# Kernel tuning notes

Measured on AMD Instinct MI355X. Metric: run time of the kernel, lower is better.

The kernel has to match this reference:

```python
import jax, jax.numpy as jnp
import numpy as np
from jax import lax

C = 128          # channel_size
NUM_HEAD = 2
P = 4            # local_patch_num


def setup_inputs() -> dict:
    key = jax.random.key(0)
    ks = jax.random.split(key, 16)
    def w(k, shape, scale=0.02):
        return jax.random.normal(k, shape, dtype=jnp.float32) * scale
    return dict(
        x=jax.random.normal(ks[0], (16, C, 128, 128), jnp.float32),
        h0=jax.random.normal(ks[1], (1, C, 64, 64), jnp.float32),
        c0=jax.random.normal(ks[2], (1, C, 64, 64), jnp.float32),
        conv_w=w(ks[3], (C, C, 2, 2)), conv_b=jnp.zeros((C,), jnp.float32),
        qkv1_w=w(ks[4], (3 * C, C)), qkv1_b=jnp.zeros((3 * C,), jnp.float32),
        mlp1_w1=w(ks[5], (4 * C, C)), mlp1_b1=jnp.zeros((4 * C,), jnp.float32),
        mlp1_w2=w(ks[6], (C, 4 * C)), mlp1_b2=jnp.zeros((C,), jnp.float32),
        qkv2_w=w(ks[7], (3 * C, C)), qkv2_b=jnp.zeros((3 * C,), jnp.float32),
        mlp2_w1=w(ks[8], (4 * C, C)), mlp2_b1=jnp.zeros((4 * C,), jnp.float32),
        mlp2_w2=w(ks[9], (C, 4 * C)), mlp2_b2=jnp.zeros((C,), jnp.float32),
        lstm_wx=w(ks[10], (4 * C, C)),   # 1x1 conv, no bias
        lstm_wh=w(ks[11], (4 * C, C)),   # 1x1 conv
        lstm_bh=jnp.zeros((4 * C,), jnp.float32),
    )


def _linear(x, w, b):
    # torch Linear: y = x @ W.T + b, W is [out, in]
    return jnp.einsum('...i,oi->...o', x, w) + b


def _msa(x, w, b, num_head):
    # x: [b, A, L, c]; attend over L within each group A. scale = sqrt(channel_size).
    bb, A, L, c = x.shape
    hd = c // num_head
    qkv = _linear(x, w, b).reshape(bb, A, L, 3, num_head, hd)
    q = jnp.transpose(qkv[..., 0, :, :], (0, 1, 3, 2, 4))  # [b,A,h,L,hd]
    k = jnp.transpose(qkv[..., 1, :, :], (0, 1, 3, 2, 4))
    v = jnp.transpose(qkv[..., 2, :, :], (0, 1, 3, 2, 4))
    score = jnp.einsum('bahlc,bahmc->bahlm', q, k) / (c ** 0.5)
    attn = jax.nn.softmax(score, axis=-1)
    out = jnp.einsum('bahlm,bahmc->bahlc', attn, v)
    return jnp.transpose(out, (0, 1, 3, 2, 4)).reshape(bb, A, L, c)


def _mlp(x, w1, b1, w2, b2):
    return _linear(jax.nn.gelu(_linear(x, w1, b1), approximate=False), w2, b2)


def reference(x, h0, c0, conv_w, conv_b,
              qkv1_w, qkv1_b, mlp1_w1, mlp1_b1, mlp1_w2, mlp1_b2,
              qkv2_w, qkv2_b, mlp2_w1, mlp2_b1, mlp2_w2, mlp2_b2,
              lstm_wx, lstm_wh, lstm_bh):
    # Conv2d(C, C, kernel=2, stride=2)
    x = lax.conv_general_dilated(x, conv_w, (2, 2), 'VALID',
                                 dimension_numbers=('NCHW', 'OIHW', 'NCHW'))
    x = x + conv_b[None, :, None, None]
    b, c, Hs, Ws = x.shape
    yg, xg = Hs // P, Ws // P
    # Window_partition: b c (yg yl) (xg xl) -> b (yg xg) (yl xl) c
    xw = x.reshape(b, c, yg, P, xg, P).transpose(0, 2, 4, 3, 5, 1).reshape(b, yg * xg, P * P, c)
    xw = xw + _msa(xw, qkv1_w, qkv1_b, NUM_HEAD)      # LocalMSA over window tokens
    xw = xw + _mlp(xw, mlp1_w1, mlp1_b1, mlp1_w2, mlp1_b2)
    xt = jnp.transpose(xw, (0, 2, 1, 3))              # b g l c -> b l g c
    xt = xt + _msa(xt, qkv2_w, qkv2_b, NUM_HEAD)      # DilatedMSA over windows
    xt = xt + _mlp(xt, mlp2_w1, mlp2_b1, mlp2_w2, mlp2_b2)
    # Window_reverse: b (yl xl) (yg xg) c -> b c (yg yl) (xg xl)
    xr = xt.reshape(b, P, P, yg, xg, c).transpose(0, 5, 3, 1, 4, 2).reshape(b, c, yg * P, xg * P)

    # ConvLSTM recurrence over the batch dimension (hidden carried sample-to-sample)
    def step(carry, xi):
        h, Cc = carry  # [C,H,W]
        gates = (jnp.einsum('oc,chw->ohw', lstm_wx, xi)
                 + jnp.einsum('oc,chw->ohw', lstm_wh, h)
                 + lstm_bh[:, None, None])
        f, i, s, o = jnp.split(gates, 4, axis=0)
        f = jax.nn.softmax(f, axis=0)   # Softmax2d = softmax over channels
        i = jax.nn.softmax(i, axis=0)
        o = jax.nn.softmax(o, axis=0)
        s = jnp.tanh(s)
        Cn = f * Cc + i * s
        hn = o * jnp.tanh(Cn)
        return (hn, Cn), hn

    (hf, Cf), hs = lax.scan(step, (h0[0], c0[0]), xr)
    return hs, hf[None], Cf[None]
```

## Files before the change

kernel.cpp:

```cpp
#include <hip/hip_runtime.h>
#include <hip/hip_bf16.h>

typedef unsigned int u32;
typedef unsigned short u16;

#define DI __device__ __forceinline__

typedef __attribute__((ext_vector_type(8))) __bf16 bf16x8;
typedef __attribute__((ext_vector_type(4))) float f32x4;

DI float b2f_u(u32 u){ return __uint_as_float(u << 16); }
DI u16 f2b_u(float f){
  u32 x = __float_as_uint(f);
  x += 0x7fffu + ((x >> 16) & 1u);
  return (u16)(x >> 16);
}
DI void ld8b(const u16* p, float* o){
  uint4 v = *reinterpret_cast<const uint4*>(p);
  o[0] = b2f_u(v.x & 0xffffu); o[1] = b2f_u(v.x >> 16);
  o[2] = b2f_u(v.y & 0xffffu); o[3] = b2f_u(v.y >> 16);
  o[4] = b2f_u(v.z & 0xffffu); o[5] = b2f_u(v.z >> 16);
  o[6] = b2f_u(v.w & 0xffffu); o[7] = b2f_u(v.w >> 16);
}
DI void st8b(u16* p, const float* i){
  uint4 v;
  v.x = (u32)f2b_u(i[0]) | ((u32)f2b_u(i[1]) << 16);
  v.y = (u32)f2b_u(i[2]) | ((u32)f2b_u(i[3]) << 16);
  v.z = (u32)f2b_u(i[4]) | ((u32)f2b_u(i[5]) << 16);
  v.w = (u32)f2b_u(i[6]) | ((u32)f2b_u(i[7]) << 16);
  *reinterpret_cast<uint4*>(p) = v;
}

__global__ void k_detect(const u32* __restrict__ xw, int* __restrict__ flag){
  __shared__ int cnt;
  int t = threadIdx.x;
  if (t == 0) cnt = 0;
  __syncthreads();
  int c = 0;
  for (int i = t; i < 2048; i += 256){
    u32 lo = xw[i] & 0xffffu;
    u32 e = (lo >> 7) & 0xffu;
    if (e < 100u || e > 140u) c++;
  }
  atomicAdd(&cnt, c);
  __syncthreads();
  if (t == 0) *flag = (cnt > 200) ? 1 : 0;
}

__global__ void k_prep(
  const void* __restrict__ conv_w, const void* __restrict__ qkv1_w,
  const void* __restrict__ m1w1, const void* __restrict__ m1w2,
  const void* __restrict__ qkv2_w, const void* __restrict__ m2w1, const void* __restrict__ m2w2,
  const void* __restrict__ lwx, const void* __restrict__ lwh,
  const void* __restrict__ conv_b, const void* __restrict__ qkv1_b,
  const void* __restrict__ m1b1, const void* __restrict__ m1b2,
  const void* __restrict__ qkv2_b, const void* __restrict__ m2b1, const void* __restrict__ m2b2,
  const void* __restrict__ lbh,
  u16* __restrict__ wB_conv, u16* __restrict__ wB_qkv1, u16* __restrict__ wB_m1a,
  u16* __restrict__ wB_m1b, u16* __restrict__ wB_qkv2, u16* __restrict__ wB_m2a,
  u16* __restrict__ wB_m2b, u16* __restrict__ wBx, u16* __restrict__ wBh,
  float* __restrict__ bf_conv, float* __restrict__ bf_qkv1, float* __restrict__ bf_m1b1,
  float* __restrict__ bf_m1b2, float* __restrict__ bf_qkv2, float* __restrict__ bf_m2b1,
  float* __restrict__ bf_m2b2, float* __restrict__ bf_lbh,
  const int* __restrict__ flag){
  int bid = blockIdx.x, t = threadIdx.x;
  int fl = *flag;
  auto cvb = [&](const void* s, u16* d, int base, int n){
    int i = (bid - base)*256 + t;
    if (i < n) d[i] = fl ? f2b_u(((const float*)s)[i]) : ((const u16*)s)[i];
  };
  auto ldf = [&](const void* s, int i)->float{
    return fl ? ((const float*)s)[i] : b2f_u((u32)((const u16*)s)[i]);
  };
  if (bid < 256)       cvb(conv_w, wB_conv, 0,    65536);
  else if (bid < 448)  cvb(qkv1_w, wB_qkv1, 256,  49152);
  else if (bid < 704)  cvb(m1w1,   wB_m1a,  448,  65536);
  else if (bid < 960)  cvb(m1w2,   wB_m1b,  704,  65536);
  else if (bid < 1152) cvb(qkv2_w, wB_qkv2, 960,  49152);
  else if (bid < 1408) cvb(m2w1,   wB_m2a,  1152, 65536);
  else if (bid < 1664) cvb(m2w2,   wB_m2b,  1408, 65536);
  else if (bid < 1920) cvb(lwx,    wBx,     1664, 65536);
  else if (bid < 2176) cvb(lwh,    wBh,     1920, 65536);
  else {
    int i = (bid - 2176)*256 + t;
    if (i < 128)       bf_conv[i]        = ldf(conv_b, i);
    else if (i < 512)  bf_qkv1[i-128]    = ldf(qkv1_b, i-128);
    else if (i < 1024) bf_m1b1[i-512]    = ldf(m1b1,   i-512);
    else if (i < 1152) bf_m1b2[i-1024]   = ldf(m1b2,   i-1024);
    else if (i < 1536) bf_qkv2[i-1152]   = ldf(qkv2_b, i-1152);
    else if (i < 2048) bf_m2b1[i-1536]   = ldf(m2b1,   i-1536);
    else if (i < 2176) bf_m2b2[i-2048]   = ldf(m2b2,   i-2048);
    else if (i < 2688) bf_lbh[i-2176]    = ldf(lbh,    i-2176);
  }
}

__global__ __launch_bounds__(256) void k_conv(const void* __restrict__ x_raw,
                                              const u16* __restrict__ wB,
                                              const float* __restrict__ bias, u16* __restrict__ outA,
                                              const int* __restrict__ flag){
  __shared__ __align__(16) u16 pool[128*136];
  u16* Aa = pool;
  u16* Ys = pool;
  int t = threadIdx.x, bid = blockIdx.x;
  int xh = bid & 1, yg = (bid >> 1) & 15, b = bid >> 5;
  size_t slab = (size_t)b*2097152 + (size_t)(yg*8)*128 + (size_t)xh*64;
  int w = t >> 6, lane = t & 63, fr = lane & 15, fg = lane >> 4;
  f32x4 acc[2][8];
  #pragma unroll
  for (int j=0;j<8;j++){
    float bv = bias[j*16 + fr];
    acc[0][j] = {bv,bv,bv,bv};
    acc[1][j] = {bv,bv,bv,bv};
  }
  for (int ci0 = 0; ci0 < 128; ci0 += 16){
    if (ci0) __syncthreads();
    if (*flag){
      const float* xb = (const float*)x_raw + slab + (size_t)ci0*16384;
      #pragma unroll
      for (int i=0;i<4;i++){
        int idx = i*256 + t;
        int row = idx >> 3, seg = idx & 7;
        int cr = row >> 3, py = row & 7;
        const float* sp = xb + (size_t)cr*16384 + py*128 + seg*8;
        float4 v0 = *reinterpret_cast<const float4*>(sp);
        float4 v1 = *reinterpret_cast<const float4*>(sp + 4);
        int tok0 = seg*16 + (py>>1)*4;
        int k0 = cr*4 + (py&1)*2;
        *reinterpret_cast<u32*>(&Aa[(tok0+0)*72 + k0]) = (u32)f2b_u(v0.x) | ((u32)f2b_u(v0.y)<<16);
        *reinterpret_cast<u32*>(&Aa[(tok0+1)*72 + k0]) = (u32)f2b_u(v0.z) | ((u32)f2b_u(v0.w)<<16);
        *reinterpret_cast<u32*>(&Aa[(tok0+2)*72 + k0]) = (u32)f2b_u(v1.x) | ((u32)f2b_u(v1.y)<<16);
        *reinterpret_cast<u32*>(&Aa[(tok0+3)*72 + k0]) = (u32)f2b_u(v1.z) | ((u32)f2b_u(v1.w)<<16);
      }
    } else {
      const u16* xb = (const u16*)x_raw + slab + (size_t)ci0*16384;
      #pragma unroll
      for (int i=0;i<4;i++){
        int idx = i*256 + t;
        int row = idx >> 3, seg = idx & 7;
        int cr = row >> 3, py = row & 7;
        uint4 v = *reinterpret_cast<const uint4*>(xb + (size_t)cr*16384 + py*128 + seg*8);
        int tok0 = seg*16 + (py>>1)*4;
        int k0 = cr*4 + (py&1)*2;
        *reinterpret_cast<u32*>(&Aa[(tok0+0)*72 + k0]) = v.x;
        *reinterpret_cast<u32*>(&Aa[(tok0+1)*72 + k0]) = v.y;
        *reinterpret_cast<u32*>(&Aa[(tok0+2)*72 + k0]) = v.z;
        *reinterpret_cast<u32*>(&Aa[(tok0+3)*72 + k0]) = v.w;
      }
    }
    __syncthreads();
    bf16x8 a0[2], a1[2];
    #pragma unroll
    for (int kk=0;kk<2;kk++){
      a0[kk] = *reinterpret_cast<const bf16x8*>(&Aa[(w*16+fr)*72 + kk*32 + fg*8]);
      a1[kk] = *reinterpret_cast<const bf16x8*>(&Aa[((w+4)*16+fr)*72 + kk*32 + fg*8]);
    }
    #pragma unroll
    for (int j=0;j<8;j++){
      const u16* wp = wB + (size_t)(j*16+fr)*512 + ci0*4 + fg*8;
      bf16x8 b0 = *reinterpret_cast<const bf16x8*>(wp);
      bf16x8 b1 = *reinterpret_cast<const bf16x8*>(wp + 32);
      acc[0][j] = __builtin_amdgcn_mfma_f32_16x16x32_bf16(a0[0], b0, acc[0][j], 0, 0, 0);
      acc[0][j] = __builtin_amdgcn_mfma_f32_16x16x32_bf16(a0[1], b1, acc[0][j], 0, 0, 0);
      acc[1][j] = __builtin_amdgcn_mfma_f32_16x16x32_bf16(a1[0], b0, acc[1][j], 0, 0, 0);
      acc[1][j] = __builtin_amdgcn_mfma_f32_16x16x32_bf16(a1[1], b1, acc[1][j], 0, 0, 0);
    }
  }
  __syncthreads();
  #pragma unroll
  for (int tt=0;tt<2;tt++){
    int tokbase = (w + tt*4)*16;
    #pragma unroll
    for (int j=0;j<8;j++){
      #pragma unroll
      for (int r=0;r<4;r++)
        Ys[(tokbase + fg*4 + r)*136 + j*16 + fr] = f2b_u(acc[tt][j][r]);
    }
  }
  __syncthreads();
  {
    int tok = t >> 1, half = t & 1;
    int gl = yg*16 + xh*8 + (tok >> 4);
    int l = tok & 15;
    u16* dst = outA + ((size_t)(b*256 + gl)*16 + l)*128 + half*64;
    const u16* src = &Ys[tok*136 + half*64];
    #pragma unroll
    for (int q2=0;q2<8;q2++)
      *reinterpret_cast<uint4*>(dst + q2*8) = *reinterpret_cast<const uint4*>(src + q2*8);
  }
}

__global__ __launch_bounds__(256) void k_msa1(const u16* __restrict__ A, const u16* __restrict__ wB,
                                              const float* __restrict__ qbias, u16* __restrict__ B){
  __shared__ u16 Xs[32*136];
  __shared__ float QKV[32*388];
  __shared__ float S[1024];
  int t = threadIdx.x, bid = blockIdx.x;
  {
    int l = t >> 3, c0 = (t & 7)*16;
    const u16* src = A + (size_t)bid*4096 + l*128 + c0;
    *reinterpret_cast<uint4*>(&Xs[l*136 + c0])     = *reinterpret_cast<const uint4*>(src);
    *reinterpret_cast<uint4*>(&Xs[l*136 + c0 + 8]) = *reinterpret_cast<const uint4*>(src + 8);
  }
  __syncthreads();
  {
    int w = t >> 6, lane = t & 63, fr = lane & 15, fg = lane >> 4;
    bf16x8 a0[4], a1[4];
    #pragma unroll
    for (int k=0;k<4;k++){
      a0[k] = *reinterpret_cast<const bf16x8*>(&Xs[fr*136 + k*32 + fg*8]);
      a1[k] = *reinterpret_cast<const bf16x8*>(&Xs[(16+fr)*136 + k*32 + fg*8]);
    }
    #pragma unroll
    for (int j=0;j<6;j++){
      int o = w*96 + j*16 + fr;
      float bv = qbias[o];
      f32x4 d0 = {bv,bv,bv,bv}, d1 = {bv,bv,bv,bv};
      const u16* wp = wB + (size_t)o*128 + fg*8;
      #pragma unroll
      for (int k=0;k<4;k++){
        bf16x8 b = *reinterpret_cast<const bf16x8*>(wp + k*32);
        d0 = __builtin_amdgcn_mfma_f32_16x16x32_bf16(a0[k], b, d0, 0, 0, 0);
        d1 = __builtin_amdgcn_mfma_f32_16x16x32_bf16(a1[k], b, d1, 0, 0, 0);
      }
      #pragma unroll
      for (int r=0;r<4;r++){
        QKV[(fg*4+r)*388 + o]      = d0[r];
        QKV[(16+fg*4+r)*388 + o]   = d1[r];
      }
    }
  }
  __syncthreads();
  const float scale = 0.08838834764831845f;
  for (int e = t; e < 1024; e += 256){
    int win = e >> 9, h = (e>>8)&1, l = (e>>4)&15, m = e&15;
    const float* q = &QKV[(win*16+l)*388 + h*64];
    const float* kk = &QKV[(win*16+m)*388 + 128 + h*64];
    float s = 0.f;
    #pragma unroll
    for (int d=0; d<64; d++) s += q[d]*kk[d];
    S[win*512 + (h*16+l)*16 + m] = s*scale;
  }
  __syncthreads();
  if (t < 64){
    float* row = &S[(t>>5)*512 + (t&31)*16];
    float mx = row[0];
    #pragma unroll
    for (int m=1;m<16;m++) mx = fmaxf(mx,row[m]);
    float sum = 0.f;
    #pragma unroll
    for (int m=0;m<16;m++){ float e = expf(row[m]-mx); row[m]=e; sum+=e; }
    float inv = 1.0f/sum;
    #pragma unroll
    for (int m=0;m<16;m++) row[m] *= inv;
  }
  __syncthreads();
  {
    int l32 = t >> 3, og = t & 7, o0 = og*16;
    int win = l32 >> 4, l = l32 & 15;
    float out16[16];
    #pragma unroll
    for (int j=0;j<16;j++){
      int o = o0+j, h = o >> 6, d = o & 63;
      const float* p = &S[win*512 + (h*16+l)*16];
      float s = 0.f;
      #pragma unroll
      for (int m=0;m<16;m++) s += p[m]*QKV[(win*16+m)*388 + 256 + h*64 + d];
      out16[j] = s + b2f_u((u32)Xs[l32*136 + o]);
    }
    st8b(B + (size_t)bid*4096 + l32*128 + o0, out16);
    st8b(B + (size_t)bid*4096 + l32*128 + o0 + 8, out16 + 8);
  }
}

template<int MODE>
__global__ __launch_bounds__(256) void k_mlp(const u16* __restrict__ in,
    const u16* __restrict__ w1B, const float* __restrict__ b1,
    const u16* __restrict__ w2B, const float* __restrict__ b2,
    u16* __restrict__ out){
  __shared__ u16 Xs[32*136];
  __shared__ u16 Hs[32*520];
  __shared__ u16 Ys[32*136];
  int t = threadIdx.x, bid = blockIdx.x;
  {
    int l = t >> 3, c0 = (t & 7)*16;
    const u16* src = in + (size_t)bid*4096 + l*128 + c0;
    *reinterpret_cast<uint4*>(&Xs[l*136 + c0])     = *reinterpret_cast<const uint4*>(src);
    *reinterpret_cast<uint4*>(&Xs[l*136 + c0 + 8]) = *reinterpret_cast<const uint4*>(src + 8);
  }
  __syncthreads();
  int w = t >> 6, lane = t & 63, fr = lane & 15, fg = lane >> 4;

  {
    bf16x8 a0[4], a1[4];
    #pragma unroll
    for (int k=0;k<4;k++){
      a0[k] = *reinterpret_cast<const bf16x8*>(&Xs[fr*136 + k*32 + fg*8]);
      a1[k] = *reinterpret_cast<const bf16x8*>(&Xs[(16+fr)*136 + k*32 + fg*8]);
    }
    #pragma unroll
    for (int j=0;j<8;j++){
      int o = w*128 + j*16 + fr;
      float bv = b1[o];
      f32x4 d0 = {bv,bv,bv,bv}, d1 = {bv,bv,bv,bv};
      const u16* wp = w1B + (size_t)o*128 + fg*8;
      #pragma unroll
      for (int k=0;k<4;k++){
        bf16x8 b = *reinterpret_cast<const bf16x8*>(wp + k*32);
        d0 = __builtin_amdgcn_mfma_f32_16x16x32_bf16(a0[k], b, d0, 0, 0, 0);
        d1 = __builtin_amdgcn_mfma_f32_16x16x32_bf16(a1[k], b, d1, 0, 0, 0);
      }
      #pragma unroll
      for (int r=0;r<4;r++){
        float v0 = d0[r], v1 = d1[r];
        Hs[(fg*4+r)*520 + o]      = f2b_u(0.5f*v0*(1.0f + erff(v0*0.70710678118654752f)));
        Hs[(16+fg*4+r)*520 + o]   = f2b_u(0.5f*v1*(1.0f + erff(v1*0.70710678118654752f)));
      }
    }
  }
  __syncthreads();

  {
    int na = w*32 + fr, nb = na + 16;
    float ba = b2[na], bb = b2[nb];
    f32x4 d00 = {ba,ba,ba,ba}, d01 = {bb,bb,bb,bb};
    f32x4 d10 = {ba,ba,ba,ba}, d11 = {bb,bb,bb,bb};
    const u16* wpa = w2B + (size_t)na*512 + fg*8;
    const u16* wpb = w2B + (size_t)nb*512 + fg*8;
    #pragma unroll
    for (int k=0;k<16;k++){
      bf16x8 aa = *reinterpret_cast<const bf16x8*>(&Hs[fr*520 + k*32 + fg*8]);
      bf16x8 ab = *reinterpret_cast<const bf16x8*>(&Hs[(16+fr)*520 + k*32 + fg*8]);
      bf16x8 bA = *reinterpret_cast<const bf16x8*>(wpa + k*32);
      bf16x8 bB = *reinterpret_cast<const bf16x8*>(wpb + k*32);
      d00 = __builtin_amdgcn_mfma_f32_16x16x32_bf16(aa, bA, d00, 0, 0, 0);
      d01 = __builtin_amdgcn_mfma_f32_16x16x32_bf16(aa, bB, d01, 0, 0, 0);
      d10 = __builtin_amdgcn_mfma_f32_16x16x32_bf16(ab, bA, d10, 0, 0, 0);
      d11 = __builtin_amdgcn_mfma_f32_16x16x32_bf16(ab, bB, d11, 0, 0, 0);
    }
    #pragma unroll
    for (int r=0;r<4;r++){
      int ta = fg*4 + r, tb = 16 + ta;
      Ys[ta*136 + na] = f2b_u(d00[r] + b2f_u((u32)Xs[ta*136 + na]));
      Ys[ta*136 + nb] = f2b_u(d01[r] + b2f_u((u32)Xs[ta*136 + nb]));
      Ys[tb*136 + na] = f2b_u(d10[r] + b2f_u((u32)Xs[tb*136 + na]));
      Ys[tb*136 + nb] = f2b_u(d11[r] + b2f_u((u32)Xs[tb*136 + nb]));
    }
  }
  __syncthreads();

  {
    int tok = t >> 3, oc = (t & 7)*16;
    uint4 v0 = *reinterpret_cast<const uint4*>(&Ys[tok*136 + oc]);
    uint4 v1 = *reinterpret_cast<const uint4*>(&Ys[tok*136 + oc + 8]);
    int T = bid*32 + tok;
    size_t addr;
    if (MODE == 1){
      int b = T >> 12, g = (T >> 4) & 255, ll = T & 15;
      addr = ((size_t)((b*16 + ll)*256 + g))*128 + oc;
    } else {
      int b = T >> 12, ll = (T >> 8) & 15, g = T & 255;
      int pcoord = ((g >> 4)*4 + (ll >> 2))*64 + ((g & 15)*4 + (ll & 3));
      addr = ((size_t)(b*4096 + pcoord))*128 + oc;
    }
    *reinterpret_cast<uint4*>(out + addr)     = v0;
    *reinterpret_cast<uint4*>(out + addr + 8) = v1;
  }
}

__global__ __launch_bounds__(256) void k_qkv2(const u16* __restrict__ in, const u16* __restrict__ wB,
                                              const float* __restrict__ bias,
                                              u16* __restrict__ qbuf, u16* __restrict__ kvbuf){
  __shared__ u16 Xs[32*136];
  __shared__ u16 Qs[32*392];
  int t = threadIdx.x, bid = blockIdx.x;
  {
    int l = t >> 3, c0 = (t & 7)*16;
    const u16* src = in + (size_t)bid*4096 + l*128 + c0;
    *reinterpret_cast<uint4*>(&Xs[l*136 + c0])     = *reinterpret_cast<const uint4*>(src);
    *reinterpret_cast<uint4*>(&Xs[l*136 + c0 + 8]) = *reinterpret_cast<const uint4*>(src + 8);
  }
  __syncthreads();
  {
    int w = t >> 6, lane = t & 63, fr = lane & 15, fg = lane >> 4;
    bf16x8 a0[4], a1[4];
    #pragma unroll
    for (int k=0;k<4;k++){
      a0[k] = *reinterpret_cast<const bf16x8*>(&Xs[fr*136 + k*32 + fg*8]);
      a1[k] = *reinterpret_cast<const bf16x8*>(&Xs[(16+fr)*136 + k*32 + fg*8]);
    }
    #pragma unroll
    for (int j=0;j<6;j++){
      int o = w*96 + j*16 + fr;
      float bv = bias[o];
      f32x4 d0 = {bv,bv,bv,bv}, d1 = {bv,bv,bv,bv};
      const u16* wp = wB + (size_t)o*128 + fg*8;
      #pragma unroll
      for (int k=0;k<4;k++){
        bf16x8 b = *reinterpret_cast<const bf16x8*>(wp + k*32);
        d0 = __builtin_amdgcn_mfma_f32_16x16x32_bf16(a0[k], b, d0, 0, 0, 0);
        d1 = __builtin_amdgcn_mfma_f32_16x16x32_bf16(a1[k], b, d1, 0, 0, 0);
      }
      #pragma unroll
      for (int r=0;r<4;r++){
        Qs[(fg*4+r)*392 + o]    = f2b_u(d0[r]);
        Qs[(16+fg*4+r)*392 + o] = f2b_u(d1[r]);
      }
    }
  }
  __syncthreads();
  {
    int l = t >> 3, og = t & 7, o0 = og*48;
    size_t tok = (size_t)bid*32 + l;
    #pragma unroll
    for (int m=0; m<6; m++){
      int oc = o0 + m*8;
      uint4 v = *reinterpret_cast<const uint4*>(&Qs[l*392 + oc]);
      if (oc < 128) *reinterpret_cast<uint4*>(qbuf + tok*128 + oc) = v;
      else          *reinterpret_cast<uint4*>(kvbuf + tok*256 + (oc-128)) = v;
    }
  }
}

__global__ __launch_bounds__(256) void k_attn2(const u16* __restrict__ qbuf, const u16* __restrict__ kvbuf,
                                               u16* __restrict__ y){
  __shared__ __align__(16) char pool[24064];
  u16* Qb = (u16*)pool;
  u16* Kb = (u16*)(pool + 9216);
  u16* Vt = (u16*)(pool + 13824);
  u16* Pb = (u16*)(pool + 18944);
  float* Os = (float*)pool;

  int t = threadIdx.x, bid = blockIdx.x;
  int qt = bid & 3, h = (bid >> 2) & 1, bl = bid >> 3;
  size_t tokbase = (size_t)bl * 256;
  {
    int r = t >> 2, seg = t & 3;
    const u16* src = qbuf + (tokbase + qt*64 + r)*128 + h*64 + seg*16;
    uint4 v0 = *reinterpret_cast<const uint4*>(src);
    uint4 v1 = *reinterpret_cast<const uint4*>(src + 8);
    *reinterpret_cast<uint4*>(&Qb[r*72 + seg*16])     = v0;
    *reinterpret_cast<uint4*>(&Qb[r*72 + seg*16 + 8]) = v1;
  }
  int w = t >> 6, lane = t & 63;
  int fc = lane & 15, fg = lane >> 4;
  float m_reg[4], l_reg[4];
  #pragma unroll
  for (int r=0;r<4;r++){ m_reg[r] = -1e30f; l_reg[r] = 0.0f; }
  f32x4 o[4];
  #pragma unroll
  for (int j=0;j<4;j++) o[j] = {0.f,0.f,0.f,0.f};
  const float scale = 0.08838834764831845f;

  for (int kt=0; kt<8; kt++){
    {
      int r = t >> 3, seg = t & 7;
      const u16* base = kvbuf + (tokbase + kt*32 + r)*256 + h*64;
      *reinterpret_cast<uint4*>(&Kb[r*72 + seg*8]) = *reinterpret_cast<const uint4*>(base + seg*8);
    }
    {
      int pp = t >> 4, dg = t & 15, d0 = dg*4;
      const u16* b0 = kvbuf + (tokbase + kt*32 + 2*pp)*256 + h*64 + 128 + d0;
      uint2 v0 = *reinterpret_cast<const uint2*>(b0);
      uint2 v1 = *reinterpret_cast<const uint2*>(b0 + 256);
      *reinterpret_cast<u32*>(&Vt[(d0+0)*40 + 2*pp]) = (v0.x & 0xffffu) | (v1.x << 16);
      *reinterpret_cast<u32*>(&Vt[(d0+1)*40 + 2*pp]) = (v0.x >> 16) | (v1.x & 0xffff0000u);
      *reinterpret_cast<u32*>(&Vt[(d0+2)*40 + 2*pp]) = (v0.y & 0xffffu) | (v1.y << 16);
      *reinterpret_cast<u32*>(&Vt[(d0+3)*40 + 2*pp]) = (v0.y >> 16) | (v1.y & 0xffff0000u);
    }
    __syncthreads();
    f32x4 s0 = {0.f,0.f,0.f,0.f}, s1 = {0.f,0.f,0.f,0.f};
    {
      bf16x8 a0  = *reinterpret_cast<const bf16x8*>(&Qb[(w*16+fc)*72 + fg*8]);
      bf16x8 a1  = *reinterpret_cast<const bf16x8*>(&Qb[(w*16+fc)*72 + 32 + fg*8]);
      bf16x8 b00 = *reinterpret_cast<const bf16x8*>(&Kb[fc*72 + fg*8]);
      bf16x8 b01 = *reinterpret_cast<const bf16x8*>(&Kb[fc*72 + 32 + fg*8]);
      bf16x8 b10 = *reinterpret_cast<const bf16x8*>(&Kb[(16+fc)*72 + fg*8]);
      bf16x8 b11 = *reinterpret_cast<const bf16x8*>(&Kb[(16+fc)*72 + 32 + fg*8]);
      s0 = __builtin_amdgcn_mfma_f32_16x16x32_bf16(a0, b00, s0, 0, 0, 0);
      s0 = __builtin_amdgcn_mfma_f32_16x16x32_bf16(a1, b01, s0, 0, 0, 0);
      s1 = __builtin_amdgcn_mfma_f32_16x16x32_bf16(a0, b10, s1, 0, 0, 0);
      s1 = __builtin_amdgcn_mfma_f32_16x16x32_bf16(a1, b11, s1, 0, 0, 0);
    }
    float corr[4];
    #pragma unroll
    for (int r=0;r<4;r++){
      float v0 = s0[r]*scale, v1 = s1[r]*scale;
      float mx = fmaxf(v0, v1);
      mx = fmaxf(mx, __shfl_xor(mx, 1));
      mx = fmaxf(mx, __shfl_xor(mx, 2));
      mx = fmaxf(mx, __shfl_xor(mx, 4));
      mx = fmaxf(mx, __shfl_xor(mx, 8));
      float mnew = fmaxf(m_reg[r], mx);
      corr[r] = expf(m_reg[r] - mnew);
      m_reg[r] = mnew;
      float p0 = expf(v0 - mnew), p1 = expf(v1 - mnew);
      float sum = p0 + p1;
      sum += __shfl_xor(sum, 1);
      sum += __shfl_xor(sum, 2);
      sum += __shfl_xor(sum, 4);
      sum += __shfl_xor(sum, 8);
      l_reg[r] = l_reg[r]*corr[r] + sum;
      int row = w*16 + fg*4 + r;
      Pb[row*40 + fc]      = f2b_u(p0);
      Pb[row*40 + 16 + fc] = f2b_u(p1);
    }
    {
      bf16x8 pa = *reinterpret_cast<const bf16x8*>(&Pb[(w*16+fc)*40 + fg*8]);
      #pragma unroll
      for (int jt=0;jt<4;jt++){
        bf16x8 vb = *reinterpret_cast<const bf16x8*>(&Vt[(jt*16+fc)*40 + fg*8]);
        f32x4 oo = o[jt];
        oo[0] *= corr[0]; oo[1] *= corr[1]; oo[2] *= corr[2]; oo[3] *= corr[3];
        o[jt] = __builtin_amdgcn_mfma_f32_16x16x32_bf16(pa, vb, oo, 0, 0, 0);
      }
    }
    __syncthreads();
  }
  float inv[4];
  #pragma unroll
  for (int r=0;r<4;r++) inv[r] = 1.0f / l_reg[r];
  #pragma unroll
  for (int jt=0;jt<4;jt++){
    #pragma unroll
    for (int r=0;r<4;r++)
      Os[(w*16 + fg*4 + r)*68 + jt*16 + fc] = o[jt][r] * inv[r];
  }
  __syncthreads();
  {
    int row = t >> 2, seg = t & 3;
    float ov[16];
    #pragma unroll
    for (int j=0;j<16;j++) ov[j] = Os[row*68 + seg*16 + j];
    u16* dst = y + (tokbase + qt*64 + row)*128 + h*64 + seg*16;
    float res[16]; ld8b(dst, res); ld8b(dst+8, res+8);
    float o16[16];
    #pragma unroll
    for (int j=0;j<16;j++) o16[j] = ov[j] + res[j];
    st8b(dst, o16); st8b(dst+8, o16+8);
  }
}

__global__ __launch_bounds__(512) void k_lstm_all(const u16* __restrict__ xD,
    const void* __restrict__ h0, const void* __restrict__ c0,
    const u16* __restrict__ wBx, const u16* __restrict__ wBh, const float* __restrict__ bh,
    void* __restrict__ dout, const int* __restrict__ flag){
  __shared__ u16 Xa[16*136];
  __shared__ u16 Ha[16*136];
  __shared__ float glds[4*16*132];
  __shared__ float part[4*16*132];
  __shared__ float Cls[16*132];
  __shared__ u16 hst[16*136];
  int t = threadIdx.x, bid = blockIdx.x;
  int pix0 = bid*16;
  int fl = *flag;
  if (t < 256){
    int c = t >> 1, half = t & 1;
    int pxb = half*8;
    if (fl){
      const float* hp = (const float*)h0 + (size_t)c*4096 + pix0 + pxb;
      const float* cp = (const float*)c0 + (size_t)c*4096 + pix0 + pxb;
      #pragma unroll
      for (int i=0;i<8;i++){
        Ha[(pxb+i)*136 + c] = f2b_u(hp[i]);
        Cls[(pxb+i)*132 + c] = cp[i];
      }
    } else {
      const u16* hp = (const u16*)h0 + (size_t)c*4096 + pix0 + pxb;
      const u16* cp = (const u16*)c0 + (size_t)c*4096 + pix0 + pxb;
      #pragma unroll
      for (int i=0;i<8;i++){
        Ha[(pxb+i)*136 + c] = hp[i];
        Cls[(pxb+i)*132 + c] = b2f_u((u32)cp[i]);
      }
    }
  }
  int w = t >> 6, lane = t & 63, fr = lane & 15, fg = lane >> 4;
  int g = w & 3, ks = w >> 2;
  const u16* wSel = ks ? wBh : wBx;
  const u16* aSel = ks ? Ha : Xa;
  for (int n = 0; n < 16; n++){
    if (t < 256){
      int px = t >> 4, c0v = (t & 15)*8;
      *reinterpret_cast<uint4*>(&Xa[px*136 + c0v]) =
        *reinterpret_cast<const uint4*>(xD + ((size_t)n*4096 + pix0 + px)*128 + c0v);
    }
    __syncthreads();
    f32x4 acc[8];
    {
      bf16x8 a[4];
      #pragma unroll
      for (int k=0;k<4;k++)
        a[k] = *reinterpret_cast<const bf16x8*>(&aSel[fr*136 + k*32 + fg*8]);
      #pragma unroll
      for (int j=0;j<8;j++){
        int o = g*128 + j*16 + fr;
        f32x4 d;
        if (ks == 0){ float bv = bh[o]; d = {bv,bv,bv,bv}; }
        else        { d = {0.f,0.f,0.f,0.f}; }
        const u16* wp = wSel + (size_t)o*128 + fg*8;
        #pragma unroll
        for (int k=0;k<4;k++){
          bf16x8 b = *reinterpret_cast<const bf16x8*>(wp + k*32);
          d = __builtin_amdgcn_mfma_f32_16x16x32_bf16(a[k], b, d, 0, 0, 0);
        }
        acc[j] = d;
      }
    }
    if (ks == 1){
      #pragma unroll
      for (int j=0;j<8;j++)
        #pragma unroll
        for (int r=0;r<4;r++)
          part[(g*16 + fg*4 + r)*132 + j*16 + fr] = acc[j][r];
    }
    __syncthreads();
    if (ks == 0){
      #pragma unroll
      for (int j=0;j<8;j++)
        #pragma unroll
        for (int r=0;r<4;r++)
          acc[j][r] += part[(g*16 + fg*4 + r)*132 + j*16 + fr];
      if (g == 2){
        #pragma unroll
        for (int j=0;j<8;j++)
          #pragma unroll
          for (int r=0;r<4;r++)
            glds[(g*16 + fg*4 + r)*132 + j*16 + fr] = tanhf(acc[j][r]);
      } else {
        #pragma unroll
        for (int r=0;r<4;r++){
          float mx = acc[0][r];
          #pragma unroll
          for (int j=1;j<8;j++) mx = fmaxf(mx, acc[j][r]);
          mx = fmaxf(mx, __shfl_xor(mx, 1));
          mx = fmaxf(mx, __shfl_xor(mx, 2));
          mx = fmaxf(mx, __shfl_xor(mx, 4));
          mx = fmaxf(mx, __shfl_xor(mx, 8));
          float e[8], sum = 0.f;
          #pragma unroll
          for (int j=0;j<8;j++){ e[j] = expf(acc[j][r] - mx); sum += e[j]; }
          sum += __shfl_xor(sum, 1);
          sum += __shfl_xor(sum, 2);
          sum += __shfl_xor(sum, 4);
          sum += __shfl_xor(sum, 8);
          float inv = 1.0f/sum;
          #pragma unroll
          for (int j=0;j<8;j++)
            glds[(g*16 + fg*4 + r)*132 + j*16 + fr] = e[j]*inv;
        }
      }
    }
    __syncthreads();
    if (t < 256){
      int chg = t & 15, px = t >> 4;
      int ch0 = chg*8;
      float fv[8], iv[8], sv[8], ov[8], cc[8];
      #pragma unroll
      for (int q2=0;q2<2;q2++){
        *reinterpret_cast<float4*>(&fv[q2*4]) = *reinterpret_cast<const float4*>(&glds[(0*16+px)*132 + ch0 + q2*4]);
        *reinterpret_cast<float4*>(&iv[q2*4]) = *reinterpret_cast<const float4*>(&glds[(1*16+px)*132 + ch0 + q2*4]);
        *reinterpret_cast<float4*>(&sv[q2*4]) = *reinterpret_cast<const float4*>(&glds[(2*16+px)*132 + ch0 + q2*4]);
        *reinterpret_cast<float4*>(&ov[q2*4]) = *reinterpret_cast<const float4*>(&glds[(3*16+px)*132 + ch0 + q2*4]);
        *reinterpret_cast<float4*>(&cc[q2*4]) = *reinterpret_cast<const float4*>(&Cls[px*132 + ch0 + q2*4]);
      }
      float cn[8], hn[8];
      #pragma unroll
      for (int j=0;j<8;j++){
        cn[j] = fv[j]*cc[j] + iv[j]*sv[j];
        hn[j] = ov[j]*tanhf(cn[j]);
      }
      #pragma unroll
      for (int q2=0;q2<2;q2++)
        *reinterpret_cast<float4*>(&Cls[px*132 + ch0 + q2*4]) = *reinterpret_cast<const float4*>(&cn[q2*4]);
      uint4 pk;
      pk.x = (u32)f2b_u(hn[0]) | ((u32)f2b_u(hn[1]) << 16);
      pk.y = (u32)f2b_u(hn[2]) | ((u32)f2b_u(hn[3]) << 16);
      pk.z = (u32)f2b_u(hn[4]) | ((u32)f2b_u(hn[5]) << 16);
      pk.w = (u32)f2b_u(hn[6]) | ((u32)f2b_u(hn[7]) << 16);
      *reinterpret_cast<uint4*>(&Ha[px*136 + ch0])  = pk;
      *reinterpret_cast<uint4*>(&hst[px*136 + ch0]) = pk;
      if (n == 15){
        #pragma unroll
        for (int q2=0;q2<2;q2++)
          *reinterpret_cast<float4*>(&glds[px*132 + ch0 + q2*4]) = *reinterpret_cast<const float4*>(&hn[q2*4]);
      }
    }
    __syncthreads();
    if (t < 256){
      int ch = t >> 1, ph = t & 1;
      size_t ob = (size_t)n*524288 + (size_t)ch*4096 + pix0 + ph*8;
      if (fl){
        float* df = (float*)dout;
        float v[8];
        #pragma unroll
        for (int i=0;i<8;i++) v[i] = b2f_u((u32)hst[(ph*8+i)*136 + ch]);
        *reinterpret_cast<float4*>(df + ob)     = make_float4(v[0],v[1],v[2],v[3]);
        *reinterpret_cast<float4*>(df + ob + 4) = make_float4(v[4],v[5],v[6],v[7]);
      } else {
        u16* db = (u16*)dout;
        uint4 pk;
        pk.x = (u32)hst[(ph*8+0)*136 + ch] | ((u32)hst[(ph*8+1)*136 + ch] << 16);
        pk.y = (u32)hst[(ph*8+2)*136 + ch] | ((u32)hst[(ph*8+3)*136 + ch] << 16);
        pk.z = (u32)hst[(ph*8+4)*136 + ch] | ((u32)hst[(ph*8+5)*136 + ch] << 16);
        pk.w = (u32)hst[(ph*8+6)*136 + ch] | ((u32)hst[(ph*8+7)*136 + ch] << 16);
        *reinterpret_cast<uint4*>(db + ob) = pk;
      }
    }
  }
  __syncthreads();
  if (t < 256){
    int c = t >> 1, half = t & 1;
    int pxb = half*8;
    if (fl){
      float hv[8], cv[8];
      #pragma unroll
      for (int i=0;i<8;i++){ hv[i] = glds[(pxb+i)*132 + c]; cv[i] = Cls[(pxb+i)*132 + c]; }
      float* df = (float*)dout;
      size_t hb = 8388608u + (size_t)c*4096 + pix0 + pxb;
      size_t cb = 8912896u + (size_t)c*4096 + pix0 + pxb;
      *reinterpret_cast<float4*>(df + hb)     = make_float4(hv[0],hv[1],hv[2],hv[3]);
      *reinterpret_cast<float4*>(df + hb + 4) = make_float4(hv[4],hv[5],hv[6],hv[7]);
      *reinterpret_cast<float4*>(df + cb)     = make_float4(cv[0],cv[1],cv[2],cv[3]);
      *reinterpret_cast<float4*>(df + cb + 4) = make_float4(cv[4],cv[5],cv[6],cv[7]);
    } else {
      u16* db = (u16*)dout;
      uint4 hp, cp2;
      hp.x = (u32)hst[(pxb+0)*136 + c] | ((u32)hst[(pxb+1)*136 + c] << 16);
      hp.y = (u32)hst[(pxb+2)*136 + c] | ((u32)hst[(pxb+3)*136 + c] << 16);
      hp.z = (u32)hst[(pxb+4)*136 + c] | ((u32)hst[(pxb+5)*136 + c] << 16);
      hp.w = (u32)hst[(pxb+6)*136 + c] | ((u32)hst[(pxb+7)*136 + c] << 16);
      cp2.x = (u32)f2b_u(Cls[(pxb+0)*132 + c]) | ((u32)f2b_u(Cls[(pxb+1)*132 + c]) << 16);
      cp2.y = (u32)f2b_u(Cls[(pxb+2)*132 + c]) | ((u32)f2b_u(Cls[(pxb+3)*132 + c]) << 16);
      cp2.z = (u32)f2b_u(Cls[(pxb+4)*132 + c]) | ((u32)f2b_u(Cls[(pxb+5)*132 + c]) << 16);
      cp2.w = (u32)f2b_u(Cls[(pxb+6)*132 + c]) | ((u32)f2b_u(Cls[(pxb+7)*132 + c]) << 16);
      *reinterpret_cast<uint4*>(db + 8388608u + (size_t)c*4096 + pix0 + pxb) = hp;
      *reinterpret_cast<uint4*>(db + 8912896u + (size_t)c*4096 + pix0 + pxb) = cp2;
    }
  }
}

extern "C" void kernel_launch(void* const* d_in, const int* in_sizes, int n_in,
                              void* d_out, int out_size, void* d_ws, size_t ws_size,
                              hipStream_t stream) {
  const void* x      = d_in[0];
  const void* h0     = d_in[1];
  const void* c0     = d_in[2];
  const void* conv_w = d_in[3];
  const void* conv_b = d_in[4];
  const void* qkv1_w = d_in[5];
  const void* qkv1_b = d_in[6];
  const void* m1w1   = d_in[7];
  const void* m1b1   = d_in[8];
  const void* m1w2   = d_in[9];
  const void* m1b2   = d_in[10];
  const void* qkv2_w = d_in[11];
  const void* qkv2_b = d_in[12];
  const void* m2w1   = d_in[13];
  const void* m2b1   = d_in[14];
  const void* m2w2   = d_in[15];
  const void* m2b2   = d_in[16];
  const void* lwx    = d_in[17];
  const void* lwh    = d_in[18];
  const void* lbh    = d_in[19];

  char* p = (char*)d_ws;
  auto alloc = [&](size_t bytes)->void*{
    void* r = (void*)p; p += (bytes + 255) & ~(size_t)255; return r;
  };
  int*   flag    = (int*)alloc(256);
  u16* wB_conv = (u16*)alloc(128*512*2);
  u16* wB_qkv1 = (u16*)alloc(384*128*2);
  u16* wB_m1a  = (u16*)alloc(512*128*2);
  u16* wB_m1b  = (u16*)alloc(128*512*2);
  u16* wB_qkv2 = (u16*)alloc(384*128*2);
  u16* wB_m2a  = (u16*)alloc(512*128*2);
  u16* wB_m2b  = (u16*)alloc(128*512*2);
  u16* wBx     = (u16*)alloc(512*128*2);
  u16* wBh     = (u16*)alloc(512*128*2);
  float* bf_conv = (float*)alloc(128*4);
  float* bf_qkv1 = (float*)alloc(384*4);
  float* bf_m1b1 = (float*)alloc(512*4);
  float* bf_m1b2 = (float*)alloc(128*4);
  float* bf_qkv2 = (float*)alloc(384*4);
  float* bf_m2b1 = (float*)alloc(512*4);
  float* bf_m2b2 = (float*)alloc(128*4);
  float* bf_lbh  = (float*)alloc(512*4);
  u16* R0   = (u16*)alloc(16777216);
  u16* Rbig = (u16*)alloc(33554432);

  u16* bufA = R0;
  u16* bufB = Rbig;
  u16* bufC = R0;
  u16* qbuf = (u16*)d_out;
  u16* kvbuf = Rbig;
  u16* bufD = Rbig;

  k_detect<<<1, 256, 0, stream>>>((const u32*)x, flag);

  k_prep<<<2187, 256, 0, stream>>>(
      conv_w, qkv1_w, m1w1, m1w2, qkv2_w, m2w1, m2w2, lwx, lwh,
      conv_b, qkv1_b, m1b1, m1b2, qkv2_b, m2b1, m2b2, lbh,
      wB_conv, wB_qkv1, wB_m1a, wB_m1b, wB_qkv2, wB_m2a, wB_m2b,
      wBx, wBh,
      bf_conv, bf_qkv1, bf_m1b1, bf_m1b2, bf_qkv2, bf_m2b1, bf_m2b2, bf_lbh,
      flag);

  k_conv<<<512, 256, 0, stream>>>(x, wB_conv, bf_conv, bufA, flag);
  k_msa1<<<2048, 256, 0, stream>>>(bufA, wB_qkv1, bf_qkv1, bufB);
  k_mlp<1><<<2048, 256, 0, stream>>>(bufB, wB_m1a, bf_m1b1, wB_m1b, bf_m1b2, bufC);
  k_qkv2<<<2048, 256, 0, stream>>>(bufC, wB_qkv2, bf_qkv2, qbuf, kvbuf);
  k_attn2<<<2048, 256, 0, stream>>>(qbuf, kvbuf, bufC);
  k_mlp<2><<<2048, 256, 0, stream>>>(bufC, wB_m2a, bf_m2b1, wB_m2b, bf_m2b2, bufD);

  k_lstm_all<<<256, 512, 0, stream>>>(bufD, h0, c0, wBx, wBh, bf_lbh, d_out, flag);
}
```

Measured before the change: 661.1 us.

## Fuse local MSA and first MLP into one kernel with shared-memory handoff

Merges the local window attention kernel and the following MLP kernel into a single kernel. The attention output is kept in shared memory (bf16) and fed directly to the MLP GEMMs, and the MLP result is written out in the transposed layout that the next kernel expects. This removes one kernel launch and a full global round-trip of the intermediate activation. In exchange, shared memory per block grows to about 61 KB through an aliased pool, which can lower occupancy.

```diff
diff --git a/kernel.cpp b/kernel.cpp
--- a/kernel.cpp
+++ b/kernel.cpp
@@ -189,11 +189,18 @@
   }
 }
 
-__global__ __launch_bounds__(256) void k_msa1(const u16* __restrict__ A, const u16* __restrict__ wB,
-                                              const float* __restrict__ qbias, u16* __restrict__ B){
-  __shared__ u16 Xs[32*136];
-  __shared__ float QKV[32*388];
-  __shared__ float S[1024];
+__global__ __launch_bounds__(256) void k_msa1mlp(const u16* __restrict__ A, const u16* __restrict__ wB,
+    const float* __restrict__ qbias,
+    const u16* __restrict__ w1B, const float* __restrict__ b1,
+    const u16* __restrict__ w2B, const float* __restrict__ b2,
+    u16* __restrict__ out){
+  __shared__ __align__(16) char pool[62464];
+  u16*  Xs  = (u16*)pool;
+  float* QKV = (float*)(pool + 8704);
+  float* S   = (float*)(pool + 58368);
+  u16*  X2  = (u16*)(pool + 8704);
+  u16*  Hs  = (u16*)(pool + 17408);
+  u16*  Ys  = (u16*)(pool + 50688);
   int t = threadIdx.x, bid = blockIdx.x;
   {
     int l = t >> 3, c0 = (t & 7)*16;
@@ -202,8 +209,8 @@
     *reinterpret_cast<uint4*>(&Xs[l*136 + c0 + 8]) = *reinterpret_cast<const uint4*>(src + 8);
   }
   __syncthreads();
-  {
-    int w = t >> 6, lane = t & 63, fr = lane & 15, fg = lane >> 4;
+  int w = t >> 6, lane = t & 63, fr = lane & 15, fg = lane >> 4;
+  {
     bf16x8 a0[4], a1[4];
     #pragma unroll
     for (int k=0;k<4;k++){
@@ -254,21 +261,92 @@
     for (int m=0;m<16;m++) row[m] *= inv;
   }
   __syncthreads();
-  {
-    int l32 = t >> 3, og = t & 7, o0 = og*16;
-    int win = l32 >> 4, l = l32 & 15;
-    float out16[16];
+  float out16[16];
+  int l32o = t >> 3, ogo = t & 7, o0o = ogo*16;
+  {
+    int win = l32o >> 4, l = l32o & 15;
     #pragma unroll
     for (int j=0;j<16;j++){
-      int o = o0+j, h = o >> 6, d = o & 63;
+      int o = o0o+j, h = o >> 6, d = o & 63;
       const float* p = &S[win*512 + (h*16+l)*16];
       float s = 0.f;
       #pragma unroll
       for (int m=0;m<16;m++) s += p[m]*QKV[(win*16+m)*388 + 256 + h*64 + d];
-      out16[j] = s + b2f_u((u32)Xs[l32*136 + o]);
-    }
-    st8b(B + (size_t)bid*4096 + l32*128 + o0, out16);
-    st8b(B + (size_t)bid*4096 + l32*128 + o0 + 8, out16 + 8);
+      out16[j] = s + b2f_u((u32)Xs[l32o*136 + o]);
+    }
+  }
+  __syncthreads();
+  #pragma unroll
+  for (int j=0;j<16;j++) X2[l32o*136 + o0o + j] = f2b_u(out16[j]);
+  __syncthreads();
+
+  {
+    bf16x8 a0[4], a1[4];
+    #pragma unroll
+    for (int k=0;k<4;k++){
+      a0[k] = *reinterpret_cast<const bf16x8*>(&X2[fr*136 + k*32 + fg*8]);
+      a1[k] = *reinterpret_cast<const bf16x8*>(&X2[(16+fr)*136 + k*32 + fg*8]);
+    }
+    #pragma unroll
+    for (int j=0;j<8;j++){
+      int o = w*128 + j*16 + fr;
+      float bv = b1[o];
+      f32x4 d0 = {bv,bv,bv,bv}, d1 = {bv,bv,bv,bv};
+      const u16* wp = w1B + (size_t)o*128 + fg*8;
+      #pragma unroll
+      for (int k=0;k<4;k++){
+        bf16x8 b = *reinterpret_cast<const bf16x8*>(wp + k*32);
+        d0 = __builtin_amdgcn_mfma_f32_16x16x32_bf16(a0[k], b, d0, 0, 0, 0);
+        d1 = __builtin_amdgcn_mfma_f32_16x16x32_bf16(a1[k], b, d1, 0, 0, 0);
+      }
+      #pragma unroll
+      for (int r=0;r<4;r++){
+        float v0 = d0[r], v1 = d1[r];
+        Hs[(fg*4+r)*520 + o]      = f2b_u(0.5f*v0*(1.0f + erff(v0*0.70710678118654752f)));
+        Hs[(16+fg*4+r)*520 + o]   = f2b_u(0.5f*v1*(1.0f + erff(v1*0.70710678118654752f)));
+      }
+    }
+  }
+  __syncthreads();
+
+  {
+    int na = w*32 + fr, nb = na + 16;
+    float ba = b2[na], bb = b2[nb];
+    f32x4 d00 = {ba,ba,ba,ba}, d01 = {bb,bb,bb,bb};
+    f32x4 d10 = {ba,ba,ba,ba}, d11 = {bb,bb,bb,bb};
+    const u16* wpa = w2B + (size_t)na*512 + fg*8;
+    const u16* wpb = w2B + (size_t)nb*512 + fg*8;
+    #pragma unroll
+    for (int k=0;k<16;k++){
+      bf16x8 aa = *reinterpret_cast<const bf16x8*>(&Hs[fr*520 + k*32 + fg*8]);
+      bf16x8 ab = *reinterpret_cast<const bf16x8*>(&Hs[(16+fr)*520 + k*32 + fg*8]);
+      bf16x8 bA = *reinterpret_cast<const bf16x8*>(wpa + k*32);
+      bf16x8 bB = *reinterpret_cast<const bf16x8*>(wpb + k*32);
+      d00 = __builtin_amdgcn_mfma_f32_16x16x32_bf16(aa, bA, d00, 0, 0, 0);
+      d01 = __builtin_amdgcn_mfma_f32_16x16x32_bf16(aa, bB, d01, 0, 0, 0);
+      d10 = __builtin_amdgcn_mfma_f32_16x16x32_bf16(ab, bA, d10, 0, 0, 0);
+      d11 = __builtin_amdgcn_mfma_f32_16x16x32_bf16(ab, bB, d11, 0, 0, 0);
+    }
+    #pragma unroll
+    for (int r=0;r<4;r++){
+      int ta = fg*4 + r, tb = 16 + ta;
+      Ys[ta*136 + na] = f2b_u(d00[r] + b2f_u((u32)X2[ta*136 + na]));
+      Ys[ta*136 + nb] = f2b_u(d01[r] + b2f_u((u32)X2[ta*136 + nb]));
+      Ys[tb*136 + na] = f2b_u(d10[r] + b2f_u((u32)X2[tb*136 + na]));
+      Ys[tb*136 + nb] = f2b_u(d11[r] + b2f_u((u32)X2[tb*136 + nb]));
+    }
+  }
+  __syncthreads();
+
+  {
+    int tok = t >> 3, oc = (t & 7)*16;
+    uint4 v0 = *reinterpret_cast<const uint4*>(&Ys[tok*136 + oc]);
+    uint4 v1 = *reinterpret_cast<const uint4*>(&Ys[tok*136 + oc + 8]);
+    int T = bid*32 + tok;
+    int b = T >> 12, g = (T >> 4) & 255, ll = T & 15;
+    size_t addr = ((size_t)((b*16 + ll)*256 + g))*128 + oc;
+    *reinterpret_cast<uint4*>(out + addr)     = v0;
+    *reinterpret_cast<uint4*>(out + addr + 8) = v1;
   }
 }
 
@@ -789,7 +867,6 @@
   u16* Rbig = (u16*)alloc(33554432);
 
   u16* bufA = R0;
-  u16* bufB = Rbig;
   u16* bufC = R0;
   u16* qbuf = (u16*)d_out;
   u16* kvbuf = Rbig;
@@ -806,8 +883,8 @@
       flag);
 
   k_conv<<<512, 256, 0, stream>>>(x, wB_conv, bf_conv, bufA, flag);
-  k_msa1<<<2048, 256, 0, stream>>>(bufA, wB_qkv1, bf_qkv1, bufB);
-  k_mlp<1><<<2048, 256, 0, stream>>>(bufB, wB_m1a, bf_m1b1, wB_m1b, bf_m1b2, bufC);
+  k_msa1mlp<<<2048, 256, 0, stream>>>(bufA, wB_qkv1, bf_qkv1,
+                                      wB_m1a, bf_m1b1, wB_m1b, bf_m1b2, bufC);
   k_qkv2<<<2048, 256, 0, stream>>>(bufC, wB_qkv2, bf_qkv2, qbuf, kvbuf);
   k_attn2<<<2048, 256, 0, stream>>>(qbuf, kvbuf, bufC);
   k_mlp<2><<<2048, 256, 0, stream>>>(bufC, wB_m2a, bf_m2b1, wB_m2b, bf_m2b2, bufD);
```

Measured after the change: 687.3 us. 1.04x slower.
